# Kernel optimization log

Measured on AMD Instinct MI355X. Metric: run time of the kernel, lower is better.

## Reference

```python
import jax, jax.numpy as jnp
import numpy as np

TEMPERATURE = 2.0
SOFT_LAMBDA = 0.5
SMOOTH_L1_BETA = 1.0  # CFG.smooth_l1_beta (torch default)
EPS_COS = 1e-8
EPS_LOG = 1e-7


def _offdiag(x):
    # x: [n, n] -> [n, n-1], dropping the diagonal, preserving column order.
    n = x.shape[0]
    cols = jnp.arange(n - 1)
    idx = cols[None, :] + (cols[None, :] >= jnp.arange(n)[:, None])
    return x[jnp.arange(n)[:, None], idx]


def _cos_pair_diff(v):
    # 1 - pairwise cosine similarity, norms clamped at eps (torch CosineSimilarity).
    nv = jnp.maximum(jnp.linalg.norm(v, axis=-1), EPS_COS)
    cos = (v @ v.T) / (nv[:, None] * nv[None, :])
    return 1.0 - cos


def setup_inputs() -> dict:
    key = jax.random.key(0)
    k1, k2, k3, k4, k5 = jax.random.split(key, 5)
    n, d_feat = 384, 128
    return {
        "trans_feat": jax.random.normal(k1, (n, d_feat), dtype=jnp.float32),
        "rot_green": jax.random.normal(k2, (n, 3), dtype=jnp.float32),
        "rot_red": jax.random.normal(k3, (n, 3), dtype=jnp.float32),
        "trans": jax.random.normal(k4, (n, 3), dtype=jnp.float32),
        "sym": jax.random.randint(k5, (n, 1), 0, 2, dtype=jnp.int32),
    }


def reference(trans_feat, rot_green, rot_red, trans, sym):
    n = trans_feat.shape[0]

    # ---- label differences ----
    # trans: smooth-L1 over pairwise diffs, mean over coord dim -> [n, n]
    d = trans[:, None, :] - trans[None, :, :]
    ad = jnp.abs(d)
    sl1 = jnp.where(ad < SMOOTH_L1_BETA, 0.5 * d * d / SMOOTH_L1_BETA, ad - 0.5 * SMOOTH_L1_BETA)
    trans_diff = sl1.mean(-1)

    g = _cos_pair_diff(rot_green)
    r = _cos_pair_diff(rot_red)
    sym_mask = sym[:, 0] == 1
    pair_sym = sym_mask[:, None] | sym_mask[None, :]
    rot_diff = jnp.where(pair_sym, g, g + r)

    # ---- feature similarity logits (negative L2, zero-safe norm) ----
    fd = trans_feat[:, None, :] - trans_feat[None, :, :]
    sq = jnp.sum(fd * fd, axis=-1)
    norm = jnp.where(sq > 0, jnp.sqrt(jnp.where(sq > 0, sq, 1.0)), 0.0)
    logits = -norm / TEMPERATURE
    logits = logits - jnp.max(logits, axis=1, keepdims=True)
    exp_logits = jnp.exp(logits)

    lo = _offdiag(logits)      # [n, n-1]
    eo = _offdiag(exp_logits)  # [n, n-1]
    td = _offdiag(trans_diff)  # [n, n-1]
    rd = _offdiag(rot_diff)    # [n, n-1]

    # rank masks: mask[i, j, k] = diff[i, j] <= diff[i, k]
    trans_mask = td[:, :, None] <= td[:, None, :]
    hard_mask = trans_mask & (rd[:, :, None] <= rd[:, None, :])

    den_trans = jnp.einsum('ijk,ik->ij', trans_mask.astype(lo.dtype), eo)
    den_hard = jnp.einsum('ijk,ik->ij', hard_mask.astype(lo.dtype), eo)

    pos_trans = lo - jnp.log(den_trans + EPS_LOG)
    pos_hard = lo - jnp.log(den_hard + EPS_LOG)

    denom = n * (n - 1)
    loss_hard = -jnp.sum(pos_hard) / denom
    loss_trans = -jnp.sum(pos_trans) / denom
    return loss_hard + SOFT_LAMBDA * loss_trans
```

## Files before the change

kernel.cpp:

```cpp
#include <hip/hip_runtime.h>
#include <math.h>

#define N 384
#define DF 128
#define TI 16
#define TK 16
#define TEMP 2.0f
#define SOFT_LAMBDA 0.5f
#define BETA 1.0f
#define EPS_COS 1e-8f
#define EPS_LOG 1e-7f

__global__ __launch_bounds__(256) void rnc_pairs(
    const float* __restrict__ feat,
    const float* __restrict__ rg,
    const float* __restrict__ rr,
    const float* __restrict__ tr,
    const int*   __restrict__ sym,
    float4* __restrict__ pk)
{
    const int i0 = blockIdx.y * TI;
    const int k0 = blockIdx.x * TK;
    const int t = threadIdx.x;

    __shared__ __align__(16) float4 fi_s[TI][DF / 4 + 1];
    __shared__ __align__(16) float4 fk_s[TK][DF / 4 + 1];
    __shared__ float4 hi_s[TI], gi_s[TI], ri_s[TI];
    __shared__ float4 hk_s[TK], gk_s[TK], rk_s[TK];

    if (t < TI) {
        int g = i0 + t;
        hi_s[t] = make_float4(tr[g * 3], tr[g * 3 + 1], tr[g * 3 + 2],
                              (sym[g] == 1) ? 1.f : 0.f);
        float a = rg[g * 3], b = rg[g * 3 + 1], c = rg[g * 3 + 2];
        gi_s[t] = make_float4(a, b, c, fmaxf(sqrtf(a * a + b * b + c * c), EPS_COS));
        float d = rr[g * 3], e = rr[g * 3 + 1], f = rr[g * 3 + 2];
        ri_s[t] = make_float4(d, e, f, fmaxf(sqrtf(d * d + e * e + f * f), EPS_COS));
    } else if (t >= 32 && t < 32 + TK) {
        int g = k0 + (t - 32);
        int tl = t - 32;
        hk_s[tl] = make_float4(tr[g * 3], tr[g * 3 + 1], tr[g * 3 + 2],
                               (sym[g] == 1) ? 1.f : 0.f);
        float a = rg[g * 3], b = rg[g * 3 + 1], c = rg[g * 3 + 2];
        gk_s[tl] = make_float4(a, b, c, fmaxf(sqrtf(a * a + b * b + c * c), EPS_COS));
        float d = rr[g * 3], e = rr[g * 3 + 1], f = rr[g * 3 + 2];
        rk_s[tl] = make_float4(d, e, f, fmaxf(sqrtf(d * d + e * e + f * f), EPS_COS));
    }

    const float4* feat4 = reinterpret_cast<const float4*>(feat);
#pragma unroll
    for (int idx = 0; idx < 2; ++idx) {
        int u = t + idx * 256;
        int row = u >> 5, c = u & 31;
        fi_s[row][c] = feat4[(i0 + row) * (DF / 4) + c];
        fk_s[row][c] = feat4[(k0 + row) * (DF / 4) + c];
    }
    __syncthreads();

    const int ii = t >> 4, kk = t & 15;
    float sq = 0.f;
#pragma unroll
    for (int d = 0; d < DF / 4; ++d) {
        float4 a = fi_s[ii][d];
        float4 b = fk_s[kk][d];
        float dx = a.x - b.x, dy = a.y - b.y, dz = a.z - b.z, dw = a.w - b.w;
        sq += dx * dx + dy * dy + dz * dz + dw * dw;
    }
    const int gi = i0 + ii, gk = k0 + kk;
    float dist = (sq > 0.f) ? sqrtf(sq) : 0.f;
    float lo = -dist * (1.0f / TEMP);
    float eo = (gi == gk) ? 0.f : expf(lo);

    float4 ha = hi_s[ii], hb = hk_s[kk];
    float s = 0.f;
    {
        float d0 = ha.x - hb.x, d1 = ha.y - hb.y, d2 = ha.z - hb.z;
        float a0 = fabsf(d0), a1 = fabsf(d1), a2 = fabsf(d2);
        s += (a0 < BETA) ? (0.5f * d0 * d0 / BETA) : (a0 - 0.5f * BETA);
        s += (a1 < BETA) ? (0.5f * d1 * d1 / BETA) : (a1 - 0.5f * BETA);
        s += (a2 < BETA) ? (0.5f * d2 * d2 / BETA) : (a2 - 0.5f * BETA);
    }
    float td = s * (1.0f / 3.0f);

    float4 ga = gi_s[ii], gb = gk_s[kk];
    float gdiff = 1.0f - (ga.x * gb.x + ga.y * gb.y + ga.z * gb.z) / (ga.w * gb.w);
    float4 ra = ri_s[ii], rb = rk_s[kk];
    float rdiff = 1.0f - (ra.x * rb.x + ra.y * rb.y + ra.z * rb.z) / (ra.w * rb.w);
    bool pair_sym = (ha.w != 0.f) || (hb.w != 0.f);
    float rd = pair_sym ? gdiff : (gdiff + rdiff);

    pk[gi * N + gk] = make_float4(td, rd, eo, lo);
}

__global__ __launch_bounds__(512) void rnc_rank(
    const float4* __restrict__ pk,
    float* __restrict__ partial_h,
    float* __restrict__ partial_t)
{
    const int i = blockIdx.x >> 1;
    const int h = blockIdx.x & 1;
    const int t = threadIdx.x;

    __shared__ __align__(16) float4 pks[N];
    __shared__ __align__(16) float2 dp[192][8];
    __shared__ float red_h[8], red_t[8];

    if (t < N) pks[t] = pk[i * N + t];
    __syncthreads();

    const int w = t >> 6, l = t & 63;
    const int jl = l * 3;
    float tdj[3], rdj[3];
    float dent[3] = {0.f, 0.f, 0.f};
    float denh[3] = {0.f, 0.f, 0.f};
#pragma unroll
    for (int jj = 0; jj < 3; ++jj) {
        float4 p = pks[h * 192 + jl + jj];
        tdj[jj] = p.x;
        rdj[jj] = p.y;
    }
    const int k0 = w * 48;
#pragma unroll 4
    for (int k = k0; k < k0 + 48; ++k) {
        float4 p = pks[k];
#pragma unroll
        for (int jj = 0; jj < 3; ++jj) {
            bool mt = p.x >= tdj[jj];
            bool mh = mt && (p.y >= rdj[jj]);
            dent[jj] += mt ? p.z : 0.f;
            denh[jj] += mh ? p.z : 0.f;
        }
    }
#pragma unroll
    for (int jj = 0; jj < 3; ++jj) dp[jl + jj][w] = make_float2(dent[jj], denh[jj]);
    __syncthreads();

    float pos_h = 0.f, pos_t = 0.f;
    if (t < 192) {
        const int j = h * 192 + t;
        if (j != i) {
            float st_ = 0.f, sh_ = 0.f;
#pragma unroll
            for (int g = 0; g < 8; ++g) {
                float2 v = dp[t][g];
                st_ += v.x;
                sh_ += v.y;
            }
            float lo = pks[j].w;
            pos_h = lo - logf(sh_ + EPS_LOG);
            pos_t = lo - logf(st_ + EPS_LOG);
        }
    }
#pragma unroll
    for (int off = 32; off > 0; off >>= 1) {
        pos_h += __shfl_down(pos_h, off, 64);
        pos_t += __shfl_down(pos_t, off, 64);
    }
    if (l == 0) {
        red_h[w] = pos_h;
        red_t[w] = pos_t;
    }
    __syncthreads();
    if (t == 0) {
        float sh = 0.f, st = 0.f;
#pragma unroll
        for (int g = 0; g < 8; ++g) {
            sh += red_h[g];
            st += red_t[g];
        }
        partial_h[blockIdx.x] = sh;
        partial_t[blockIdx.x] = st;
    }
}

__global__ __launch_bounds__(768) void rnc_final(
    const float* __restrict__ partial_h,
    const float* __restrict__ partial_t,
    float* __restrict__ out)
{
    const int t = threadIdx.x;
    float hsum = partial_h[t];
    float tsum = partial_t[t];
#pragma unroll
    for (int off = 32; off > 0; off >>= 1) {
        hsum += __shfl_down(hsum, off, 64);
        tsum += __shfl_down(tsum, off, 64);
    }
    __shared__ float rh[12], rt[12];
    const int wave = t >> 6, lane = t & 63;
    if (lane == 0) {
        rh[wave] = hsum;
        rt[wave] = tsum;
    }
    __syncthreads();
    if (t == 0) {
        double sh = 0.0, st = 0.0;
#pragma unroll
        for (int w = 0; w < 12; ++w) {
            sh += (double)rh[w];
            st += (double)rt[w];
        }
        const double denom = (double)N * (double)(N - 1);
        out[0] = (float)(-(sh + (double)SOFT_LAMBDA * st) / denom);
    }
}

extern "C" void kernel_launch(void* const* d_in, const int* in_sizes, int n_in,
                              void* d_out, int out_size, void* d_ws, size_t ws_size,
                              hipStream_t stream) {
    const float* feat = (const float*)d_in[0];
    const float* rg   = (const float*)d_in[1];
    const float* rr   = (const float*)d_in[2];
    const float* tr   = (const float*)d_in[3];
    const int*   sym  = (const int*)d_in[4];
    float* out = (float*)d_out;

    float4* pk = (float4*)d_ws;
    float* partial_h = (float*)((char*)d_ws + (size_t)N * N * sizeof(float4));
    float* partial_t = partial_h + 2 * N;

    dim3 gridA(N / TK, N / TI);
    rnc_pairs<<<gridA, 256, 0, stream>>>(feat, rg, rr, tr, sym, pk);
    rnc_rank<<<2 * N, 512, 0, stream>>>(pk, partial_h, partial_t);
    rnc_final<<<1, 2 * N, 0, stream>>>(partial_h, partial_t, out);
}
```

Measured before the change: 78.95 us.

## Fuse pair computation into rank kernel, one block per row

Merges the pairwise-feature kernel and the rank kernel into one kernel with one block per row i. Each block computes its row of distances, exp-logits and label diffs directly into shared memory, so the N×N float4 intermediate never goes through global memory and one launch is removed. Each thread now handles six j columns instead of three, and the grid shrinks from 768 blocks to 384. Feature rows for k are read straight from global memory without tiling, so feature reuse relies on cache, and the smaller grid may leave compute units less occupied.

Measured after the change: 86.44 us. +9.5%, slower.

```diff
diff --git a/kernel.cpp b/kernel.cpp
--- a/kernel.cpp
+++ b/kernel.cpp
@@ -3,128 +3,94 @@
 
 #define N 384
 #define DF 128
-#define TI 16
-#define TK 16
+#define NF4 (DF / 4)
 #define TEMP 2.0f
 #define SOFT_LAMBDA 0.5f
 #define BETA 1.0f
 #define EPS_COS 1e-8f
 #define EPS_LOG 1e-7f
 
-__global__ __launch_bounds__(256) void rnc_pairs(
+__global__ __launch_bounds__(512, 4) void rnc_fused(
     const float* __restrict__ feat,
     const float* __restrict__ rg,
     const float* __restrict__ rr,
     const float* __restrict__ tr,
     const int*   __restrict__ sym,
-    float4* __restrict__ pk)
+    float* __restrict__ partial_h,
+    float* __restrict__ partial_t)
 {
-    const int i0 = blockIdx.y * TI;
-    const int k0 = blockIdx.x * TK;
+    const int i = blockIdx.x;
     const int t = threadIdx.x;
 
-    __shared__ __align__(16) float4 fi_s[TI][DF / 4 + 1];
-    __shared__ __align__(16) float4 fk_s[TK][DF / 4 + 1];
-    __shared__ float4 hi_s[TI], gi_s[TI], ri_s[TI];
-    __shared__ float4 hk_s[TK], gk_s[TK], rk_s[TK];
-
-    if (t < TI) {
-        int g = i0 + t;
-        hi_s[t] = make_float4(tr[g * 3], tr[g * 3 + 1], tr[g * 3 + 2],
-                              (sym[g] == 1) ? 1.f : 0.f);
-        float a = rg[g * 3], b = rg[g * 3 + 1], c = rg[g * 3 + 2];
-        gi_s[t] = make_float4(a, b, c, fmaxf(sqrtf(a * a + b * b + c * c), EPS_COS));
-        float d = rr[g * 3], e = rr[g * 3 + 1], f = rr[g * 3 + 2];
-        ri_s[t] = make_float4(d, e, f, fmaxf(sqrtf(d * d + e * e + f * f), EPS_COS));
-    } else if (t >= 32 && t < 32 + TK) {
-        int g = k0 + (t - 32);
-        int tl = t - 32;
-        hk_s[tl] = make_float4(tr[g * 3], tr[g * 3 + 1], tr[g * 3 + 2],
-                               (sym[g] == 1) ? 1.f : 0.f);
-        float a = rg[g * 3], b = rg[g * 3 + 1], c = rg[g * 3 + 2];
-        gk_s[tl] = make_float4(a, b, c, fmaxf(sqrtf(a * a + b * b + c * c), EPS_COS));
-        float d = rr[g * 3], e = rr[g * 3 + 1], f = rr[g * 3 + 2];
-        rk_s[tl] = make_float4(d, e, f, fmaxf(sqrtf(d * d + e * e + f * f), EPS_COS));
-    }
+    __shared__ __align__(16) float4 fi_s[NF4];
+    __shared__ __align__(16) float4 pks[N];
+    __shared__ __align__(16) float2 dp[8][N + 4];
+    __shared__ float red_h[8], red_t[8];
 
     const float4* feat4 = reinterpret_cast<const float4*>(feat);
-#pragma unroll
-    for (int idx = 0; idx < 2; ++idx) {
-        int u = t + idx * 256;
-        int row = u >> 5, c = u & 31;
-        fi_s[row][c] = feat4[(i0 + row) * (DF / 4) + c];
-        fk_s[row][c] = feat4[(k0 + row) * (DF / 4) + c];
+    if (t < NF4) fi_s[t] = feat4[i * NF4 + t];
+
+    const float tix = tr[i * 3 + 0], tiy = tr[i * 3 + 1], tiz = tr[i * 3 + 2];
+    const float gix = rg[i * 3 + 0], giy = rg[i * 3 + 1], giz = rg[i * 3 + 2];
+    const float rix = rr[i * 3 + 0], riy = rr[i * 3 + 1], riz = rr[i * 3 + 2];
+    const float ngi = fmaxf(sqrtf(gix * gix + giy * giy + giz * giz), EPS_COS);
+    const float nri = fmaxf(sqrtf(rix * rix + riy * riy + riz * riz), EPS_COS);
+    const bool symi = (sym[i] == 1);
+    __syncthreads();
+
+    if (t < N) {
+        const int k = t;
+        float sq = 0.f;
+#pragma unroll 4
+        for (int d = 0; d < NF4; ++d) {
+            float4 a = fi_s[d];
+            float4 b = feat4[k * NF4 + d];
+            float dx = a.x - b.x, dy = a.y - b.y, dz = a.z - b.z, dw = a.w - b.w;
+            sq += dx * dx + dy * dy + dz * dz + dw * dw;
+        }
+        float dist = (sq > 0.f) ? sqrtf(sq) : 0.f;
+        float lo = -dist * (1.0f / TEMP);
+        float eo = (k == i) ? 0.f : expf(lo);
+
+        float d0 = tix - tr[k * 3 + 0];
+        float d1 = tiy - tr[k * 3 + 1];
+        float d2 = tiz - tr[k * 3 + 2];
+        float a0 = fabsf(d0), a1 = fabsf(d1), a2 = fabsf(d2);
+        float s = 0.f;
+        s += (a0 < BETA) ? (0.5f * d0 * d0 / BETA) : (a0 - 0.5f * BETA);
+        s += (a1 < BETA) ? (0.5f * d1 * d1 / BETA) : (a1 - 0.5f * BETA);
+        s += (a2 < BETA) ? (0.5f * d2 * d2 / BETA) : (a2 - 0.5f * BETA);
+        float td = s * (1.0f / 3.0f);
+
+        float gkx = rg[k * 3 + 0], gky = rg[k * 3 + 1], gkz = rg[k * 3 + 2];
+        float ngk = fmaxf(sqrtf(gkx * gkx + gky * gky + gkz * gkz), EPS_COS);
+        float gd = 1.0f - (gix * gkx + giy * gky + giz * gkz) / (ngi * ngk);
+        float rkx = rr[k * 3 + 0], rky = rr[k * 3 + 1], rkz = rr[k * 3 + 2];
+        float nrk = fmaxf(sqrtf(rkx * rkx + rky * rky + rkz * rkz), EPS_COS);
+        float rdif = 1.0f - (rix * rkx + riy * rky + riz * rkz) / (nri * nrk);
+        bool ps = symi || (sym[k] == 1);
+        float rd = ps ? gd : (gd + rdif);
+
+        pks[k] = make_float4(td, rd, eo, lo);
     }
     __syncthreads();
 
-    const int ii = t >> 4, kk = t & 15;
-    float sq = 0.f;
+    const int w = t >> 6, l = t & 63;
+    float tdj[6], rdj[6], dent[6], denh[6];
 #pragma unroll
-    for (int d = 0; d < DF / 4; ++d) {
-        float4 a = fi_s[ii][d];
-        float4 b = fk_s[kk][d];
-        float dx = a.x - b.x, dy = a.y - b.y, dz = a.z - b.z, dw = a.w - b.w;
-        sq += dx * dx + dy * dy + dz * dz + dw * dw;
-    }
-    const int gi = i0 + ii, gk = k0 + kk;
-    float dist = (sq > 0.f) ? sqrtf(sq) : 0.f;
-    float lo = -dist * (1.0f / TEMP);
-    float eo = (gi == gk) ? 0.f : expf(lo);
-
-    float4 ha = hi_s[ii], hb = hk_s[kk];
-    float s = 0.f;
-    {
-        float d0 = ha.x - hb.x, d1 = ha.y - hb.y, d2 = ha.z - hb.z;
-        float a0 = fabsf(d0), a1 = fabsf(d1), a2 = fabsf(d2);
-        s += (a0 < BETA) ? (0.5f * d0 * d0 / BETA) : (a0 - 0.5f * BETA);
-        s += (a1 < BETA) ? (0.5f * d1 * d1 / BETA) : (a1 - 0.5f * BETA);
-        s += (a2 < BETA) ? (0.5f * d2 * d2 / BETA) : (a2 - 0.5f * BETA);
-    }
-    float td = s * (1.0f / 3.0f);
-
-    float4 ga = gi_s[ii], gb = gk_s[kk];
-    float gdiff = 1.0f - (ga.x * gb.x + ga.y * gb.y + ga.z * gb.z) / (ga.w * gb.w);
-    float4 ra = ri_s[ii], rb = rk_s[kk];
-    float rdiff = 1.0f - (ra.x * rb.x + ra.y * rb.y + ra.z * rb.z) / (ra.w * rb.w);
-    bool pair_sym = (ha.w != 0.f) || (hb.w != 0.f);
-    float rd = pair_sym ? gdiff : (gdiff + rdiff);
-
-    pk[gi * N + gk] = make_float4(td, rd, eo, lo);
-}
-
-__global__ __launch_bounds__(512) void rnc_rank(
-    const float4* __restrict__ pk,
-    float* __restrict__ partial_h,
-    float* __restrict__ partial_t)
-{
-    const int i = blockIdx.x >> 1;
-    const int h = blockIdx.x & 1;
-    const int t = threadIdx.x;
-
-    __shared__ __align__(16) float4 pks[N];
-    __shared__ __align__(16) float2 dp[192][8];
-    __shared__ float red_h[8], red_t[8];
-
-    if (t < N) pks[t] = pk[i * N + t];
-    __syncthreads();
-
-    const int w = t >> 6, l = t & 63;
-    const int jl = l * 3;
-    float tdj[3], rdj[3];
-    float dent[3] = {0.f, 0.f, 0.f};
-    float denh[3] = {0.f, 0.f, 0.f};
-#pragma unroll
-    for (int jj = 0; jj < 3; ++jj) {
-        float4 p = pks[h * 192 + jl + jj];
+    for (int jj = 0; jj < 6; ++jj) {
+        float4 p = pks[l + 64 * jj];
         tdj[jj] = p.x;
         rdj[jj] = p.y;
+        dent[jj] = 0.f;
+        denh[jj] = 0.f;
     }
     const int k0 = w * 48;
 #pragma unroll 4
     for (int k = k0; k < k0 + 48; ++k) {
         float4 p = pks[k];
 #pragma unroll
-        for (int jj = 0; jj < 3; ++jj) {
+        for (int jj = 0; jj < 6; ++jj) {
             bool mt = p.x >= tdj[jj];
             bool mh = mt && (p.y >= rdj[jj]);
             dent[jj] += mt ? p.z : 0.f;
@@ -132,24 +98,22 @@
         }
     }
 #pragma unroll
-    for (int jj = 0; jj < 3; ++jj) dp[jl + jj][w] = make_float2(dent[jj], denh[jj]);
+    for (int jj = 0; jj < 6; ++jj)
+        dp[w][l + 64 * jj] = make_float2(dent[jj], denh[jj]);
     __syncthreads();
 
     float pos_h = 0.f, pos_t = 0.f;
-    if (t < 192) {
-        const int j = h * 192 + t;
-        if (j != i) {
-            float st_ = 0.f, sh_ = 0.f;
+    if (t < N && t != i) {
+        float st_ = 0.f, sh_ = 0.f;
 #pragma unroll
-            for (int g = 0; g < 8; ++g) {
-                float2 v = dp[t][g];
-                st_ += v.x;
-                sh_ += v.y;
-            }
-            float lo = pks[j].w;
-            pos_h = lo - logf(sh_ + EPS_LOG);
-            pos_t = lo - logf(st_ + EPS_LOG);
+        for (int g = 0; g < 8; ++g) {
+            float2 v = dp[g][t];
+            st_ += v.x;
+            sh_ += v.y;
         }
+        float lo = pks[t].w;
+        pos_h = lo - logf(sh_ + EPS_LOG);
+        pos_t = lo - logf(st_ + EPS_LOG);
     }
 #pragma unroll
     for (int off = 32; off > 0; off >>= 1) {
@@ -168,12 +132,12 @@
             sh += red_h[g];
             st += red_t[g];
         }
-        partial_h[blockIdx.x] = sh;
-        partial_t[blockIdx.x] = st;
+        partial_h[i] = sh;
+        partial_t[i] = st;
     }
 }
 
-__global__ __launch_bounds__(768) void rnc_final(
+__global__ __launch_bounds__(N) void rnc_final(
     const float* __restrict__ partial_h,
     const float* __restrict__ partial_t,
     float* __restrict__ out)
@@ -186,7 +150,7 @@
         hsum += __shfl_down(hsum, off, 64);
         tsum += __shfl_down(tsum, off, 64);
     }
-    __shared__ float rh[12], rt[12];
+    __shared__ float rh[6], rt[6];
     const int wave = t >> 6, lane = t & 63;
     if (lane == 0) {
         rh[wave] = hsum;
@@ -196,7 +160,7 @@
     if (t == 0) {
         double sh = 0.0, st = 0.0;
 #pragma unroll
-        for (int w = 0; w < 12; ++w) {
+        for (int w = 0; w < 6; ++w) {
             sh += (double)rh[w];
             st += (double)rt[w];
         }
@@ -215,12 +179,9 @@
     const int*   sym  = (const int*)d_in[4];
     float* out = (float*)d_out;
 
-    float4* pk = (float4*)d_ws;
-    float* partial_h = (float*)((char*)d_ws + (size_t)N * N * sizeof(float4));
-    float* partial_t = partial_h + 2 * N;
+    float* partial_h = (float*)d_ws;
+    float* partial_t = partial_h + N;
 
-    dim3 gridA(N / TK, N / TI);
-    rnc_pairs<<<gridA, 256, 0, stream>>>(feat, rg, rr, tr, sym, pk);
-    rnc_rank<<<2 * N, 512, 0, stream>>>(pk, partial_h, partial_t);
-    rnc_final<<<1, 2 * N, 0, stream>>>(partial_h, partial_t, out);
+    rnc_fused<<<N, 512, 0, stream>>>(feat, rg, rr, tr, sym, partial_h, partial_t);
+    rnc_final<<<1, N, 0, stream>>>(partial_h, partial_t, out);
 }
```
